# Kernel optimization log

Hardware: AMD Instinct MI355X
Metric: run time of the kernel (lower is better)

Reference implementation:

```python
import jax, jax.numpy as jnp
import numpy as np

N, E, B = 65536, 524288, 256
FEAT, EMB, NH, NB, NC = 64, 128, 4, 2, 4
OUT = EMB // NH
SLOPE = 0.01  # LeakyReLU negative_slope used everywhere in the module


def lrelu(x):
    return jnp.where(x > 0, x, SLOPE * x)


def seg_softmax(logits, seg, nseg, mask):
    # PyG softmax(src, batch): exp(x - segment_max) / (segment_sum + 1e-16)
    z = jnp.where(mask, logits, -jnp.inf)
    m = jax.ops.segment_max(z, seg, num_segments=nseg)
    m = jnp.where(jnp.isfinite(m), m, 0.0)
    e = jnp.exp(z - m[seg])
    s = jax.ops.segment_sum(e, seg, num_segments=nseg)
    return e / (s[seg] + 1e-16)


def topk_pool(x, seg, w, min_score, nseg):
    # PyG TopKPooling with min_score: score = softmax(x.w, batch);
    # keep nodes with score > min(min_score, per-graph max - 1e-7); x_out = x*score.
    score = x @ w  # [N]
    sm = seg_softmax(score, seg, nseg, jnp.ones(score.shape, bool))
    smax = jax.ops.segment_max(sm, seg, num_segments=nseg)
    thr = jnp.minimum(smax - 1e-7, min_score)
    keep = sm > thr[seg]
    xp = jnp.where(keep[:, None], x * sm[:, None], 0.0)
    return xp, keep


def graph_conv_max(x, src, dst, emask, Wrel, Wroot, b, n):
    # PyG GraphConv(aggr='max'): out = Wrel @ max_{j in N(i)} x_j + Wroot @ x_i + b
    msg = jnp.where(emask[:, None], x[src], -jnp.inf)  # [E, d]
    agg = jax.ops.segment_max(msg, dst, num_segments=n)
    agg = jnp.where(jnp.isfinite(agg), agg, 0.0)  # nodes with no in-edges -> 0 (PyG scatter fill)
    return agg @ Wrel.T + x @ Wroot.T + b


def batchnorm(x, g, b):
    # training-mode BatchNorm1d: batch statistics, biased variance, eps=1e-5
    mu = x.mean(0)
    var = x.var(0)
    return g * (x - mu) * jax.lax.rsqrt(var + 1e-5) + b


def setup_inputs() -> dict:
    key = jax.random.key(0)
    ks = jax.random.split(key, 16)
    s_feat = np.float32(1.0 / np.sqrt(FEAT))
    s_emb = np.float32(1.0 / np.sqrt(EMB))
    return {
        "x": jax.random.normal(ks[0], (N, FEAT), jnp.float32),
        "edge_index": jax.random.randint(ks[1], (2, E), 0, N, jnp.int32),
        "batch": (jnp.arange(N, dtype=jnp.int32) // (N // B)).astype(jnp.int32),
        "W_rel0": jax.random.normal(ks[2], (EMB, FEAT), jnp.float32) * s_feat,
        "W_root0": jax.random.normal(ks[3], (EMB, FEAT), jnp.float32) * s_feat,
        "b0": jnp.zeros((EMB,), jnp.float32),
        "bn0_g": jnp.ones((EMB,), jnp.float32),
        "bn0_b": jnp.zeros((EMB,), jnp.float32),
        "blk_pool_w": jax.random.normal(ks[4], (NB, NH, EMB), jnp.float32) * s_emb,
        "blk_Wrel": jax.random.normal(ks[5], (NB, NH, OUT, EMB), jnp.float32) * s_emb,
        "blk_Wroot": jax.random.normal(ks[6], (NB, NH, OUT, EMB), jnp.float32) * s_emb,
        "blk_b": jnp.zeros((NB, NH, OUT), jnp.float32),
        "blk_bn_g": jnp.ones((NB, EMB), jnp.float32),
        "blk_bn_b": jnp.zeros((NB, EMB), jnp.float32),
        "cls_pool_w": jax.random.normal(ks[7], (NC, EMB), jnp.float32) * s_emb,
        "cls_gW1": jax.random.normal(ks[8], (NC, EMB, EMB), jnp.float32) * s_emb,
        "cls_gb1": jnp.zeros((NC, EMB), jnp.float32),
        "cls_gW2": jax.random.normal(ks[9], (NC, EMB), jnp.float32) * s_emb,
        "cls_gb2": jnp.zeros((NC,), jnp.float32),
        "cls_fW1": jax.random.normal(ks[10], (NC, EMB, EMB), jnp.float32) * s_emb,
        "cls_fb1": jnp.zeros((NC, EMB), jnp.float32),
        "cls_fW2": jax.random.normal(ks[11], (NC, EMB), jnp.float32) * s_emb,
        "cls_fb2": jnp.zeros((NC,), jnp.float32),
        "batch_size": B,
    }


def reference(x, edge_index, batch, W_rel0, W_root0, b0, bn0_g, bn0_b,
              blk_pool_w, blk_Wrel, blk_Wroot, blk_b, blk_bn_g, blk_bn_b,
              cls_pool_w, cls_gW1, cls_gb1, cls_gW2, cls_gb2,
              cls_fW1, cls_fb1, cls_fW2, cls_fb2, batch_size):
    n = x.shape[0]
    src, dst = edge_index[0], edge_index[1]
    all_e = jnp.ones(src.shape, bool)
    # conv0 -> leaky_relu -> bn0
    h = lrelu(graph_conv_max(x, src, dst, all_e, W_rel0, W_root0, b0, n))
    cur = batchnorm(h, bn0_g, bn0_b)
    # multi-head blocks: pool (min_score=0.7) -> GraphConv(max) per head, scatter
    # back to original node slots, concat heads, bn, residual 0.5*(x + 0.5*bn(new))
    for bi in range(NB):
        heads = []
        for hi in range(NH):
            xp, keep = topk_pool(cur, batch, blk_pool_w[bi, hi], 0.7, batch_size)
            emask = keep[src] & keep[dst]
            o = lrelu(graph_conv_max(xp, src, dst, emask,
                                     blk_Wrel[bi, hi], blk_Wroot[bi, hi],
                                     blk_b[bi, hi], n))
            heads.append(jnp.where(keep[:, None], o, 0.0))
        new = batchnorm(jnp.concatenate(heads, axis=-1), blk_bn_g[bi], blk_bn_b[bi])
        cur = 0.5 * (cur + 0.5 * new)
    # classification heads: pool (min_score=0.8) -> GlobalAttention -> MLP -> 1
    outs = []
    for c in range(NC):
        xp, keep = topk_pool(cur, batch, cls_pool_w[c], 0.8, batch_size)
        gate = lrelu(xp @ cls_gW1[c].T + cls_gb1[c]) @ cls_gW2[c] + cls_gb2[c]  # [N]
        a = seg_softmax(gate, batch, batch_size, keep)
        pooled = jax.ops.segment_sum(a[:, None] * xp, batch, num_segments=batch_size)  # [B, EMB]
        y = lrelu(pooled @ cls_fW1[c].T + cls_fb1[c]) @ cls_fW2[c] + cls_fb2[c]  # [B]
        outs.append(y)
    logits = jnp.stack(outs, axis=-1)  # [B, NC]
    return jax.nn.log_softmax(logits, axis=-1)
```

## Files before the change

kernel.cpp:

```cpp
#include <hip/hip_runtime.h>
#include <math.h>

#define NN 65536
#define NE 524288
#define NG 256
#define SLOPE 0.01f

__device__ __forceinline__ float lrelu(float v){ return v > 0.f ? v : SLOPE*v; }

__device__ __forceinline__ float blockMax4(float v, float* s4){
  #pragma unroll
  for(int o=32;o>0;o>>=1) v = fmaxf(v, __shfl_down(v, o, 64));
  int t = threadIdx.x;
  __syncthreads();
  if((t&63)==0) s4[t>>6] = v;
  __syncthreads();
  return fmaxf(fmaxf(s4[0], s4[1]), fmaxf(s4[2], s4[3]));
}
__device__ __forceinline__ float blockSum4(float v, float* s4){
  #pragma unroll
  for(int o=32;o>0;o>>=1) v += __shfl_down(v, o, 64);
  int t = threadIdx.x;
  __syncthreads();
  if((t&63)==0) s4[t>>6] = v;
  __syncthreads();
  return (s4[0]+s4[1])+(s4[2]+s4[3]);
}

__global__ __launch_bounds__(256) void k_count(const int* __restrict__ ei, int* __restrict__ deg){
  int e = blockIdx.x*256 + threadIdx.x;
  if(e < NE) atomicAdd(&deg[ei[NE + e]], 1);
}

__global__ __launch_bounds__(1024) void k_scan(const int* __restrict__ deg,
      int* __restrict__ offs, int* __restrict__ cursor){
  __shared__ int part[1024];
  int t = threadIdx.x;
  int base = t*64;
  int s=0;
  for(int i=0;i<64;i++) s += deg[base+i];
  part[t]=s;
  __syncthreads();
  for(int off=1; off<1024; off<<=1){
    int v = (t>=off)? part[t-off] : 0;
    __syncthreads();
    part[t] += v;
    __syncthreads();
  }
  int run = (t==0)? 0 : part[t-1];
  for(int i=0;i<64;i++){
    int d = deg[base+i];
    offs[base+i] = run; cursor[base+i] = run;
    run += d;
  }
  if(t==1023) offs[NN] = run;
}

__global__ __launch_bounds__(256) void k_scatter(const int* __restrict__ ei,
      int* __restrict__ cursor, int* __restrict__ csr){
  int e = blockIdx.x*256 + threadIdx.x;
  if(e < NE){
    int d = ei[NE + e];
    int p = atomicAdd(&cursor[d], 1);
    csr[p] = ei[e];
  }
}

__global__ __launch_bounds__(256) void k_agg0(const float* __restrict__ x,
    const int* __restrict__ offs, const int* __restrict__ csr, float* __restrict__ agg0){
  int tid = blockIdx.x*256 + threadIdx.x;
  int node = tid>>4, q = tid&15;
  int e0 = offs[node], e1 = offs[node+1];
  float4 acc = make_float4(0.f,0.f,0.f,0.f);
  if(e0 < e1){
    acc = make_float4(-INFINITY,-INFINITY,-INFINITY,-INFINITY);
    int e = e0;
    for(; e+3 < e1; e += 4){
      int s0 = csr[e], s1 = csr[e+1], s2 = csr[e+2], s3 = csr[e+3];
      float4 v0 = ((const float4*)x)[s0*16 + q];
      float4 v1 = ((const float4*)x)[s1*16 + q];
      float4 v2 = ((const float4*)x)[s2*16 + q];
      float4 v3 = ((const float4*)x)[s3*16 + q];
      acc.x=fmaxf(acc.x,fmaxf(fmaxf(v0.x,v1.x),fmaxf(v2.x,v3.x)));
      acc.y=fmaxf(acc.y,fmaxf(fmaxf(v0.y,v1.y),fmaxf(v2.y,v3.y)));
      acc.z=fmaxf(acc.z,fmaxf(fmaxf(v0.z,v1.z),fmaxf(v2.z,v3.z)));
      acc.w=fmaxf(acc.w,fmaxf(fmaxf(v0.w,v1.w),fmaxf(v2.w,v3.w)));
    }
    for(; e < e1; e++){
      int s0 = csr[e];
      float4 v0 = ((const float4*)x)[s0*16 + q];
      acc.x=fmaxf(acc.x,v0.x); acc.y=fmaxf(acc.y,v0.y);
      acc.z=fmaxf(acc.z,v0.z); acc.w=fmaxf(acc.w,v0.w);
    }
  }
  ((float4*)agg0)[node*16 + q] = acc;
}

__global__ __launch_bounds__(256, 2) void k_conv0mm(
    const float* __restrict__ agg0, const float* __restrict__ x,
    const float* __restrict__ Wrel, const float* __restrict__ Wroot,
    const float* __restrict__ b0, float* __restrict__ cur,
    float* __restrict__ bnsum, float* __restrict__ bnsq){
  __shared__ float4 As[2048];
  __shared__ float4 Ws[2048];
  const int t = threadIdx.x;
  const int tn = t & 15;
  const int tc = t >> 4;
  float acc[8][8];
  #pragma unroll
  for(int i=0;i<8;i++)
    #pragma unroll
    for(int j=0;j<8;j++) acc[i][j]=0.f;

  const size_t tileoff = (size_t)blockIdx.x * 8192;
  #pragma unroll 1
  for(int ch=0; ch<2; ch++){
    const float4* gA = (const float4*)((ch==0? agg0 : x) + tileoff);
    const float4* gW = (const float4*)(ch==0? Wrel : Wroot);
    __syncthreads();
    #pragma unroll
    for(int i=0;i<8;i++){
      int idx = t + i*256;
      int n = idx>>4, k4 = idx&15;
      int sw = n*16 + ((k4 + (n>>3))&15);
      As[sw] = gA[idx];
      Ws[sw] = gW[idx];
    }
    __syncthreads();
    #pragma unroll 4
    for(int k4=0;k4<16;k4++){
      float4 a4[8], w4[8];
      #pragma unroll
      for(int i=0;i<8;i++) a4[i] = As[(tn*8+i)*16 + ((k4+tn)&15)];
      #pragma unroll
      for(int i=0;i<8;i++) w4[i] = Ws[(tc*8+i)*16 + ((k4+tc)&15)];
      #pragma unroll
      for(int i=0;i<8;i++)
        #pragma unroll
        for(int j=0;j<8;j++){
          acc[i][j] = fmaf(a4[i].x, w4[j].x, acc[i][j]);
          acc[i][j] = fmaf(a4[i].y, w4[j].y, acc[i][j]);
          acc[i][j] = fmaf(a4[i].z, w4[j].z, acc[i][j]);
          acc[i][j] = fmaf(a4[i].w, w4[j].w, acc[i][j]);
        }
    }
  }

  float bj[8];
  #pragma unroll
  for(int j=0;j<8;j++) bj[j] = b0[tc*8+j];
  float cs[8], cq[8];
  #pragma unroll
  for(int j=0;j<8;j++){ cs[j]=0.f; cq[j]=0.f; }
  const int nbase = blockIdx.x*128;
  #pragma unroll
  for(int i=0;i<8;i++){
    int node = nbase + tn*8 + i;
    float v[8];
    #pragma unroll
    for(int j=0;j<8;j++){
      v[j] = lrelu(acc[i][j] + bj[j]);
      cs[j] += v[j]; cq[j] += v[j]*v[j];
    }
    float4 o0 = make_float4(v[0],v[1],v[2],v[3]);
    float4 o1 = make_float4(v[4],v[5],v[6],v[7]);
    ((float4*)cur)[node*32 + tc*2 + 0] = o0;
    ((float4*)cur)[node*32 + tc*2 + 1] = o1;
  }
  __syncthreads();
  float* reds = (float*)As;
  float* redq = (float*)Ws;
  #pragma unroll
  for(int j=0;j<8;j++){
    reds[(tc*8+j)*16 + tn] = cs[j];
    redq[(tc*8+j)*16 + tn] = cq[j];
  }
  __syncthreads();
  if(t<128){
    float S=0.f, Q=0.f;
    #pragma unroll
    for(int i=0;i<16;i++){ S += reds[t*16+i]; Q += redq[t*16+i]; }
    atomicAdd(&bnsum[t], S);
    atomicAdd(&bnsq[t], Q);
  }
}

template<int MODE>
__global__ __launch_bounds__(256) void k_stream(
    float* __restrict__ cur, const float* __restrict__ onew,
    const unsigned char* __restrict__ keepin,
    const float* __restrict__ bnsA, const float* __restrict__ bnqA,
    const float* __restrict__ g1, const float* __restrict__ b1,
    const float* __restrict__ bns0, const float* __restrict__ bnq0,
    const float* __restrict__ g0, const float* __restrict__ b0bn,
    const float* __restrict__ pw, float* __restrict__ scores){
  __shared__ __align__(16) float w[4][128];
  __shared__ __align__(16) float sc1[128], of1[128], sc0[128], of0[128];
  const int t = threadIdx.x;
  if(t<128){
    if(MODE>=1){
      float mu = bnsA[t]*(1.0f/NN);
      float var = bnqA[t]*(1.0f/NN) - mu*mu;
      float s = g1[t]*rsqrtf(var+1e-5f);
      sc1[t]=s; of1[t]=b1[t]-mu*s;
    }
    if(MODE<=1){
      float mu0 = bns0[t]*(1.0f/NN);
      float var0 = bnq0[t]*(1.0f/NN) - mu0*mu0;
      float s0 = g0[t]*rsqrtf(var0+1e-5f);
      sc0[t]=s0; of0[t]=b0bn[t]-mu0*s0;
    }
  }
  __syncthreads();
  for(int i=t;i<512;i+=256){
    float wv = pw[i];
    if(MODE==0) wv *= sc0[i&127];
    w[i>>7][i&127]=wv;
  }
  __syncthreads();
  const int tid = blockIdx.x*256 + t;
  const int n = tid>>5, k = tid&31;
  float4 v = ((const float4*)cur)[tid];
  if(MODE>=1){
    const int h = k>>3;
    float4 nv = make_float4(0.f,0.f,0.f,0.f);
    if((keepin[n]>>h)&1) nv = ((const float4*)onew)[tid];
    float4 s1 = *(const float4*)&sc1[k*4];
    float4 o1 = *(const float4*)&of1[k*4];
    if(MODE==1){
      float4 s0 = *(const float4*)&sc0[k*4];
      float4 o0 = *(const float4*)&of0[k*4];
      v.x = 0.5f*(s0.x*v.x+o0.x) + 0.25f*(s1.x*nv.x+o1.x);
      v.y = 0.5f*(s0.y*v.y+o0.y) + 0.25f*(s1.y*nv.y+o1.y);
      v.z = 0.5f*(s0.z*v.z+o0.z) + 0.25f*(s1.z*nv.z+o1.z);
      v.w = 0.5f*(s0.w*v.w+o0.w) + 0.25f*(s1.w*nv.w+o1.w);
    } else {
      v.x = 0.5f*v.x + 0.25f*(s1.x*nv.x+o1.x);
      v.y = 0.5f*v.y + 0.25f*(s1.y*nv.y+o1.y);
      v.z = 0.5f*v.z + 0.25f*(s1.z*nv.z+o1.z);
      v.w = 0.5f*v.w + 0.25f*(s1.w*nv.w+o1.w);
    }
    ((float4*)cur)[tid] = v;
  }
  float sch[4];
  #pragma unroll
  for(int h2=0;h2<4;h2++){
    float4 wv = *(const float4*)&w[h2][k*4];
    sch[h2] = v.x*wv.x + v.y*wv.y + v.z*wv.z + v.w*wv.w;
  }
  #pragma unroll
  for(int o=16;o>0;o>>=1){
    #pragma unroll
    for(int h2=0;h2<4;h2++) sch[h2] += __shfl_down(sch[h2], o, 32);
  }
  if(k==0) ((float4*)scores)[n] = make_float4(sch[0],sch[1],sch[2],sch[3]);
}

__global__ __launch_bounds__(256) void k_poolsel(const float* __restrict__ scores,
    float minscore, float* __restrict__ sm4, unsigned char* __restrict__ keep,
    int* __restrict__ cnt, int* __restrict__ wl){
  __shared__ float red[4];
  const int t = threadIdx.x, g = blockIdx.x, n = g*256 + t;
  float4 s4 = ((const float4*)scores)[n];
  float scv[4] = {s4.x, s4.y, s4.z, s4.w};
  float4 smout;
  unsigned kb = 0;
  #pragma unroll 1
  for(int h=0;h<4;h++){
    float m = blockMax4(scv[h], red);
    float e = expf(scv[h]-m);
    float ssum = blockSum4(e, red);
    float sm = e/(ssum + 1e-16f);
    float smax = blockMax4(sm, red);
    float thr = fminf(smax - 1e-7f, minscore);
    ((float*)&smout)[h] = sm;
    if(sm > thr){
      kb |= (1u<<h);
      int p = atomicAdd(cnt, 1);
      wl[p] = (h<<16) | n;
    }
  }
  __syncthreads();
  ((float4*)sm4)[n] = smout;
  keep[n] = (unsigned char)kb;
}

__global__ __launch_bounds__(256) void k_blockconv(const float* __restrict__ cur,
    const int* __restrict__ offs, const int* __restrict__ csr,
    const unsigned char* __restrict__ keep, const float* __restrict__ sm4,
    const int* __restrict__ cnt, const int* __restrict__ wl,
    const float* __restrict__ Wrel, const float* __restrict__ Wroot,
    const float* __restrict__ bias,
    float* __restrict__ onew, float* __restrict__ bnsum, float* __restrict__ bnsq,
    const float* __restrict__ bns0, const float* __restrict__ bnq0,
    const float* __restrict__ g0, const float* __restrict__ b0bn, int fold){
  __shared__ __align__(16) float aggs[8][128];
  __shared__ __align__(16) float xps[8][128];
  __shared__ __align__(16) float scv[128];
  __shared__ __align__(16) float ofv[128];
  const int t = threadIdx.x, grp = t>>5, lane = t&31;
  if(t<128){
    float sv = 1.f, ov = 0.f;
    if(fold){
      float mu = bns0[t]*(1.0f/NN);
      float var = bnq0[t]*(1.0f/NN) - mu*mu;
      sv = g0[t]*rsqrtf(var+1e-5f);
      ov = b0bn[t] - mu*sv;
    }
    scv[t]=sv; ofv[t]=ov;
  }
  __syncthreads();
  const float4 s4l = *(const float4*)&scv[lane*4];
  const float4 o4l = *(const float4*)&ofv[lane*4];
  const int total = *cnt;
  for(int item = blockIdx.x*8 + grp; item < total; item += gridDim.x*8){
    const int wv = wl[item];
    const int h = wv>>16, n = wv & 0xFFFF;
    const float smn = sm4[n*4+h];
    const int e0 = offs[n], e1 = offs[n+1];
    float4 acc = make_float4(-INFINITY,-INFINITY,-INFINITY,-INFINITY);
    bool any = false;
    for(int e=e0;e<e1;e++){
      int s = csr[e];
      if((keep[s]>>h)&1){
        any = true;
        float sv = sm4[s*4+h];
        float4 v = ((const float4*)cur)[s*32 + lane];
        v.x = (v.x*s4l.x + o4l.x)*sv; v.y = (v.y*s4l.y + o4l.y)*sv;
        v.z = (v.z*s4l.z + o4l.z)*sv; v.w = (v.w*s4l.w + o4l.w)*sv;
        acc.x = fmaxf(acc.x, v.x); acc.y = fmaxf(acc.y, v.y);
        acc.z = fmaxf(acc.z, v.z); acc.w = fmaxf(acc.w, v.w);
      }
    }
    if(!any) acc = make_float4(0.f,0.f,0.f,0.f);
    *(float4*)&aggs[grp][lane*4] = acc;
    float4 xv = ((const float4*)cur)[n*32 + lane];
    xv.x = (xv.x*s4l.x + o4l.x)*smn; xv.y = (xv.y*s4l.y + o4l.y)*smn;
    xv.z = (xv.z*s4l.z + o4l.z)*smn; xv.w = (xv.w*s4l.w + o4l.w)*smn;
    *(float4*)&xps[grp][lane*4] = xv;
    const float* Wr = Wrel  + (size_t)(h*32+lane)*128;
    const float* Wo = Wroot + (size_t)(h*32+lane)*128;
    float o = bias[h*32+lane];
    for(int k=0;k<32;k++){
      float4 a  = *(const float4*)&aggs[grp][k*4];
      float4 xx = *(const float4*)&xps[grp][k*4];
      float4 wr = ((const float4*)Wr)[k];
      float4 wo = ((const float4*)Wo)[k];
      o += a.x*wr.x + a.y*wr.y + a.z*wr.z + a.w*wr.w;
      o += xx.x*wo.x + xx.y*wo.y + xx.z*wo.z + xx.w*wo.w;
    }
    o = lrelu(o);
    onew[(size_t)n*128 + h*32 + lane] = o;
    atomicAdd(&bnsum[h*32+lane], o);
    atomicAdd(&bnsq[h*32+lane], o*o);
  }
}

__global__ __launch_bounds__(256) void k_cls2(const float* __restrict__ cur,
    const float* __restrict__ scores,
    const float* __restrict__ gW1, const float* __restrict__ gb1,
    const float* __restrict__ gW2, const float* __restrict__ gb2,
    const float* __restrict__ fW1, const float* __restrict__ fb1,
    const float* __restrict__ fW2, const float* __restrict__ fb2,
    float* __restrict__ yws){
  __shared__ float red[4];
  __shared__ int keptL[256];
  __shared__ float keptS[256];
  __shared__ float gateL[256];
  __shared__ __align__(16) float xk[128];
  __shared__ __align__(16) float pooled[128];
  __shared__ int nkept;
  const int t = threadIdx.x;
  const int g = blockIdx.x >> 2, c = blockIdx.x & 3;
  const int n = g*256 + t;
  float sc = scores[n*4 + c];
  float m = blockMax4(sc, red);
  float e = expf(sc-m);
  float ssum = blockSum4(e, red);
  float sm = e/(ssum+1e-16f);
  float smax = blockMax4(sm, red);
  float thr = fminf(smax - 1e-7f, 0.8f);
  if(t==0) nkept = 0;
  __syncthreads();
  if(sm > thr){
    int p = atomicAdd(&nkept,1);
    keptL[p]=t; keptS[p]=sm;
  }
  __syncthreads();
  const int K = nkept;
  for(int k=0;k<K;k++){
    int ln = keptL[k]; float sv = keptS[k];
    if(t<32){
      float4 v = ((const float4*)(cur + (size_t)(g*256+ln)*128))[t];
      v.x*=sv; v.y*=sv; v.z*=sv; v.w*=sv;
      *(float4*)&xk[t*4] = v;
    }
    __syncthreads();
    float part = 0.f;
    if(t<128){
      const float* W = gW1 + (size_t)c*16384 + (size_t)t*128;
      float a = gb1[c*128+t];
      for(int f=0;f<32;f++){
        float4 xv = *(const float4*)&xk[f*4];
        float4 wv = ((const float4*)W)[f];
        a += xv.x*wv.x + xv.y*wv.y + xv.z*wv.z + xv.w*wv.w;
      }
      part = lrelu(a) * gW2[c*128+t];
    }
    float gs = blockSum4(part, red);
    if(t==0) gateL[k] = gs + gb2[c];
    __syncthreads();
  }
  float gv = (t<K)? gateL[t] : -INFINITY;
  float gm = blockMax4(gv, red);
  float ge = (t<K)? expf(gv-gm) : 0.f;
  float gsum = blockSum4(ge, red);
  if(t<K) gateL[t] = ge/(gsum+1e-16f);
  __syncthreads();
  if(t<128){
    float acc = 0.f;
    for(int k=0;k<K;k++)
      acc += gateL[k]*keptS[k]*cur[(size_t)(g*256+keptL[k])*128 + t];
    pooled[t]=acc;
  }
  __syncthreads();
  float part2=0.f;
  if(t<128){
    const float* F = fW1 + (size_t)c*16384 + (size_t)t*128;
    float a = fb1[c*128+t];
    for(int f=0;f<32;f++){
      float4 xv = *(const float4*)&pooled[f*4];
      float4 wv = ((const float4*)F)[f];
      a += xv.x*wv.x + xv.y*wv.y + xv.z*wv.z + xv.w*wv.w;
    }
    part2 = lrelu(a) * fW2[c*128+t];
  }
  float ysum = blockSum4(part2, red);
  if(t==0) yws[g*4+c] = ysum + fb2[c];
}

__global__ __launch_bounds__(256) void k_clsfin(const float* __restrict__ yws,
                                                float* __restrict__ out){
  const int g = threadIdx.x;
  float4 y = ((const float4*)yws)[g];
  float m = fmaxf(fmaxf(y.x,y.y), fmaxf(y.z,y.w));
  float l = logf(expf(y.x-m)+expf(y.y-m)+expf(y.z-m)+expf(y.w-m));
  float4 o = make_float4(y.x-m-l, y.y-m-l, y.z-m-l, y.w-m-l);
  ((float4*)out)[g] = o;
}

extern "C" void kernel_launch(void* const* d_in, const int* in_sizes, int n_in,
                              void* d_out, int out_size, void* d_ws, size_t ws_size,
                              hipStream_t stream){
  (void)in_sizes; (void)n_in; (void)out_size; (void)ws_size;
  const float* x     = (const float*)d_in[0];
  const int*   ei    = (const int*)d_in[1];
  const float* Wrel0 = (const float*)d_in[3];
  const float* Wroot0= (const float*)d_in[4];
  const float* b0    = (const float*)d_in[5];
  const float* bn0g  = (const float*)d_in[6];
  const float* bn0b  = (const float*)d_in[7];
  const float* bpw   = (const float*)d_in[8];
  const float* bWrel = (const float*)d_in[9];
  const float* bWroot= (const float*)d_in[10];
  const float* bbv   = (const float*)d_in[11];
  const float* bbng  = (const float*)d_in[12];
  const float* bbnb  = (const float*)d_in[13];
  const float* cpw   = (const float*)d_in[14];
  const float* gW1   = (const float*)d_in[15];
  const float* gb1   = (const float*)d_in[16];
  const float* gW2   = (const float*)d_in[17];
  const float* gb2   = (const float*)d_in[18];
  const float* fW1   = (const float*)d_in[19];
  const float* fb1   = (const float*)d_in[20];
  const float* fW2   = (const float*)d_in[21];
  const float* fb2   = (const float*)d_in[22];

  char* ws = (char*)d_ws;
  float* cur   = (float*)(ws + 0);
  float* onew  = (float*)(ws + 33554432ull);
  float* agg0  = onew;
  int*   csr   = (int*)(ws + 67108864ull);
  float* sm4   = (float*)(ws + 69206016ull);
  float* scores= sm4;
  int*   wl    = (int*)(ws + 70254592ull);
  int*   offs  = (int*)(ws + 71303168ull);
  int*   cursor= (int*)(ws + 71565568ull);
  unsigned char* keep = (unsigned char*)(ws + 71827712ull);
  char*  Z     = ws + 71893248ull;
  int*   deg   = (int*)Z;
  float* bnsum0= (float*)(Z + 262144);
  float* bnsq0 = (float*)(Z + 262656);
  float* bnA   = (float*)(Z + 263168);
  float* bqA   = (float*)(Z + 263680);
  float* bnB   = (float*)(Z + 264192);
  float* bqB   = (float*)(Z + 264704);
  int*   cnt0  = (int*)(Z + 265216);
  int*   cnt1  = (int*)(Z + 265220);
  float* yws   = (float*)(Z + 266240);

  hipMemsetAsync(Z, 0, 265224, stream);

  k_count  <<<2048,256,0,stream>>>(ei, deg);
  k_scan   <<<1,1024,0,stream>>>(deg, offs, cursor);
  k_scatter<<<2048,256,0,stream>>>(ei, cursor, csr);

  k_agg0    <<<4096,256,0,stream>>>(x, offs, csr, agg0);
  k_conv0mm <<<512,256,0,stream>>>(agg0, x, Wrel0, Wroot0, b0, cur, bnsum0, bnsq0);

  k_stream<0><<<8192,256,0,stream>>>(cur, onew, keep, bnA, bqA, bbng, bbnb,
                                     bnsum0, bnsq0, bn0g, bn0b, bpw, scores);
  k_poolsel<<<256,256,0,stream>>>(scores, 0.7f, sm4, keep, cnt0, wl);

  k_blockconv<<<256,256,0,stream>>>(cur, offs, csr, keep, sm4, cnt0, wl,
                                    bWrel, bWroot, bbv, onew, bnA, bqA,
                                    bnsum0, bnsq0, bn0g, bn0b, 1);

  k_stream<1><<<8192,256,0,stream>>>(cur, onew, keep, bnA, bqA, bbng, bbnb,
                                     bnsum0, bnsq0, bn0g, bn0b, bpw + 512, scores);
  k_poolsel<<<256,256,0,stream>>>(scores, 0.7f, sm4, keep, cnt1, wl);

  k_blockconv<<<256,256,0,stream>>>(cur, offs, csr, keep, sm4, cnt1, wl,
                                    bWrel + 16384, bWroot + 16384, bbv + 128, onew, bnB, bqB,
                                    bnsum0, bnsq0, bn0g, bn0b, 0);

  k_stream<2><<<8192,256,0,stream>>>(cur, onew, keep, bnB, bqB, bbng + 128, bbnb + 128,
                                     bnsum0, bnsq0, bn0g, bn0b, cpw, scores);

  k_cls2<<<1024,256,0,stream>>>(cur, scores, gW1, gb1, gW2, gb2,
                                fW1, fb1, fW2, fb2, yws);
  k_clsfin<<<1,256,0,stream>>>(yws, (float*)d_out);
}
```

Baseline: 405.4 us.

## Vectorize CSR scan, widen agg0 unroll, rewrite conv0 matmul with register-held weights

```diff
diff --git a/kernel.cpp b/kernel.cpp
--- a/kernel.cpp
+++ b/kernel.cpp
@@ -36,9 +36,11 @@
       int* __restrict__ offs, int* __restrict__ cursor){
   __shared__ int part[1024];
   int t = threadIdx.x;
-  int base = t*64;
+  const int4* d4 = (const int4*)(deg + t*64);
+  int4 buf[16];
   int s=0;
-  for(int i=0;i<64;i++) s += deg[base+i];
+  #pragma unroll
+  for(int i=0;i<16;i++){ buf[i]=d4[i]; s += buf[i].x+buf[i].y+buf[i].z+buf[i].w; }
   part[t]=s;
   __syncthreads();
   for(int off=1; off<1024; off<<=1){
@@ -48,10 +50,16 @@
     __syncthreads();
   }
   int run = (t==0)? 0 : part[t-1];
-  for(int i=0;i<64;i++){
-    int d = deg[base+i];
-    offs[base+i] = run; cursor[base+i] = run;
-    run += d;
+  #pragma unroll
+  for(int i=0;i<16;i++){
+    int4 d = buf[i];
+    int4 o;
+    o.x = run; run += d.x;
+    o.y = run; run += d.y;
+    o.z = run; run += d.z;
+    o.w = run; run += d.w;
+    ((int4*)(offs + t*64))[i] = o;
+    ((int4*)(cursor + t*64))[i] = o;
   }
   if(t==1023) offs[NN] = run;
 }
@@ -75,16 +83,18 @@
   if(e0 < e1){
     acc = make_float4(-INFINITY,-INFINITY,-INFINITY,-INFINITY);
     int e = e0;
-    for(; e+3 < e1; e += 4){
-      int s0 = csr[e], s1 = csr[e+1], s2 = csr[e+2], s3 = csr[e+3];
-      float4 v0 = ((const float4*)x)[s0*16 + q];
-      float4 v1 = ((const float4*)x)[s1*16 + q];
-      float4 v2 = ((const float4*)x)[s2*16 + q];
-      float4 v3 = ((const float4*)x)[s3*16 + q];
-      acc.x=fmaxf(acc.x,fmaxf(fmaxf(v0.x,v1.x),fmaxf(v2.x,v3.x)));
-      acc.y=fmaxf(acc.y,fmaxf(fmaxf(v0.y,v1.y),fmaxf(v2.y,v3.y)));
-      acc.z=fmaxf(acc.z,fmaxf(fmaxf(v0.z,v1.z),fmaxf(v2.z,v3.z)));
-      acc.w=fmaxf(acc.w,fmaxf(fmaxf(v0.w,v1.w),fmaxf(v2.w,v3.w)));
+    for(; e+7 < e1; e += 8){
+      int si[8];
+      #pragma unroll
+      for(int u=0;u<8;u++) si[u] = csr[e+u];
+      float4 v[8];
+      #pragma unroll
+      for(int u=0;u<8;u++) v[u] = ((const float4*)x)[si[u]*16 + q];
+      #pragma unroll
+      for(int u=0;u<8;u++){
+        acc.x=fmaxf(acc.x,v[u].x); acc.y=fmaxf(acc.y,v[u].y);
+        acc.z=fmaxf(acc.z,v[u].z); acc.w=fmaxf(acc.w,v[u].w);
+      }
     }
     for(; e < e1; e++){
       int s0 = csr[e];
@@ -96,93 +106,53 @@
   ((float4*)agg0)[node*16 + q] = acc;
 }
 
-__global__ __launch_bounds__(256, 2) void k_conv0mm(
+__global__ __launch_bounds__(256) void k_conv0mm(
     const float* __restrict__ agg0, const float* __restrict__ x,
     const float* __restrict__ Wrel, const float* __restrict__ Wroot,
     const float* __restrict__ b0, float* __restrict__ cur,
     float* __restrict__ bnsum, float* __restrict__ bnsq){
-  __shared__ float4 As[2048];
-  __shared__ float4 Ws[2048];
   const int t = threadIdx.x;
-  const int tn = t & 15;
-  const int tc = t >> 4;
-  float acc[8][8];
-  #pragma unroll
-  for(int i=0;i<8;i++)
+  const int j = t & 127;
+  const int s = __builtin_amdgcn_readfirstlane(t >> 7);
+  float wreg[128];
+  {
+    const float4* wr4 = (const float4*)(Wrel + (size_t)j*64);
+    const float4* wo4 = (const float4*)(Wroot + (size_t)j*64);
     #pragma unroll
-    for(int j=0;j<8;j++) acc[i][j]=0.f;
-
-  const size_t tileoff = (size_t)blockIdx.x * 8192;
+    for(int i=0;i<16;i++){
+      *(float4*)&wreg[i*4]    = wr4[i];
+      *(float4*)&wreg[64+i*4] = wo4[i];
+    }
+  }
+  const float bj = b0[j];
+  float cs = 0.f, cq = 0.f;
+  const int nbase = blockIdx.x*64 + s*32;
   #pragma unroll 1
-  for(int ch=0; ch<2; ch++){
-    const float4* gA = (const float4*)((ch==0? agg0 : x) + tileoff);
-    const float4* gW = (const float4*)(ch==0? Wrel : Wroot);
-    __syncthreads();
+  for(int it=0; it<32; it++){
+    const int node = nbase + it;
+    const float* __restrict__ ra = agg0 + (size_t)node*64;
+    const float* __restrict__ rx = x    + (size_t)node*64;
+    float a0=0.f, a1=0.f, a2=0.f, a3=0.f;
     #pragma unroll
-    for(int i=0;i<8;i++){
-      int idx = t + i*256;
-      int n = idx>>4, k4 = idx&15;
-      int sw = n*16 + ((k4 + (n>>3))&15);
-      As[sw] = gA[idx];
-      Ws[sw] = gW[idx];
-    }
-    __syncthreads();
-    #pragma unroll 4
-    for(int k4=0;k4<16;k4++){
-      float4 a4[8], w4[8];
-      #pragma unroll
-      for(int i=0;i<8;i++) a4[i] = As[(tn*8+i)*16 + ((k4+tn)&15)];
-      #pragma unroll
-      for(int i=0;i<8;i++) w4[i] = Ws[(tc*8+i)*16 + ((k4+tc)&15)];
-      #pragma unroll
-      for(int i=0;i<8;i++)
-        #pragma unroll
-        for(int j=0;j<8;j++){
-          acc[i][j] = fmaf(a4[i].x, w4[j].x, acc[i][j]);
-          acc[i][j] = fmaf(a4[i].y, w4[j].y, acc[i][j]);
-          acc[i][j] = fmaf(a4[i].z, w4[j].z, acc[i][j]);
-          acc[i][j] = fmaf(a4[i].w, w4[j].w, acc[i][j]);
-        }
-    }
-  }
-
-  float bj[8];
-  #pragma unroll
-  for(int j=0;j<8;j++) bj[j] = b0[tc*8+j];
-  float cs[8], cq[8];
-  #pragma unroll
-  for(int j=0;j<8;j++){ cs[j]=0.f; cq[j]=0.f; }
-  const int nbase = blockIdx.x*128;
-  #pragma unroll
-  for(int i=0;i<8;i++){
-    int node = nbase + tn*8 + i;
-    float v[8];
+    for(int k=0;k<64;k+=4){
+      a0 = fmaf(ra[k+0], wreg[k+0], a0);
+      a1 = fmaf(ra[k+1], wreg[k+1], a1);
+      a2 = fmaf(ra[k+2], wreg[k+2], a2);
+      a3 = fmaf(ra[k+3], wreg[k+3], a3);
+    }
     #pragma unroll
-    for(int j=0;j<8;j++){
-      v[j] = lrelu(acc[i][j] + bj[j]);
-      cs[j] += v[j]; cq[j] += v[j]*v[j];
-    }
-    float4 o0 = make_float4(v[0],v[1],v[2],v[3]);
-    float4 o1 = make_float4(v[4],v[5],v[6],v[7]);
-    ((float4*)cur)[node*32 + tc*2 + 0] = o0;
-    ((float4*)cur)[node*32 + tc*2 + 1] = o1;
-  }
-  __syncthreads();
-  float* reds = (float*)As;
-  float* redq = (float*)Ws;
-  #pragma unroll
-  for(int j=0;j<8;j++){
-    reds[(tc*8+j)*16 + tn] = cs[j];
-    redq[(tc*8+j)*16 + tn] = cq[j];
-  }
-  __syncthreads();
-  if(t<128){
-    float S=0.f, Q=0.f;
-    #pragma unroll
-    for(int i=0;i<16;i++){ S += reds[t*16+i]; Q += redq[t*16+i]; }
-    atomicAdd(&bnsum[t], S);
-    atomicAdd(&bnsq[t], Q);
-  }
+    for(int k=0;k<64;k+=4){
+      a0 = fmaf(rx[k+0], wreg[64+k+0], a0);
+      a1 = fmaf(rx[k+1], wreg[64+k+1], a1);
+      a2 = fmaf(rx[k+2], wreg[64+k+2], a2);
+      a3 = fmaf(rx[k+3], wreg[64+k+3], a3);
+    }
+    float o = lrelu((a0+a1)+(a2+a3) + bj);
+    cur[(size_t)node*128 + j] = o;
+    cs += o; cq += o*o;
+  }
+  atomicAdd(&bnsum[j], cs);
+  atomicAdd(&bnsq[j], cq);
 }
 
 template<int MODE>
@@ -506,7 +476,7 @@
   k_scatter<<<2048,256,0,stream>>>(ei, cursor, csr);
 
   k_agg0    <<<4096,256,0,stream>>>(x, offs, csr, agg0);
-  k_conv0mm <<<512,256,0,stream>>>(agg0, x, Wrel0, Wroot0, b0, cur, bnsum0, bnsq0);
+  k_conv0mm <<<1024,256,0,stream>>>(agg0, x, Wrel0, Wroot0, b0, cur, bnsum0, bnsq0);
 
   k_stream<0><<<8192,256,0,stream>>>(cur, onew, keep, bnA, bqA, bbng, bbnb,
                                      bnsum0, bnsq0, bn0g, bn0b, bpw, scores);
```

New measurement: 483.5 us. +19.3%, slower.
